# Kernel optimization log

Hardware: AMD Instinct MI355X
Metric: run time of the kernel (lower is better)

The kernel has to match this reference:

```python
import jax, jax.numpy as jnp
import numpy as np

DIM = 256; HEADS = 8; HD = 32; WS = 3; LOCAL = WS * WS; SR = 4


def _unfold(x, ws):
    # x: (B, c, H, W) -> (B, c, ws*ws, H*W), zero padding (matches nn.Unfold)
    p = ws // 2
    B, c, H, W = x.shape
    xp = jnp.pad(x, ((0, 0), (0, 0), (p, p), (p, p)))
    pat = jnp.stack([xp[:, :, i:i + H, j:j + W] for i in range(ws) for j in range(ws)], axis=2)
    return pat.reshape(B, c, ws * ws, H * W)


def _l2norm(x):
    return x / jnp.sqrt(jnp.sum(x * x, axis=-1, keepdims=True) + 1e-12)


def setup_inputs():
    key = jax.random.key(0)
    ks = jax.random.split(key, 16)
    B, H, W, C, h, d = 4, 64, 64, DIM, HEADS, HD
    N = H * W; pH, pW = H // SR, W // SR; PL = pH * pW; L = 1024
    s = 0.02
    inp = {}
    inp["x"] = jax.random.normal(ks[0], (B, N, C), jnp.float32)
    inp["relative_coords_table"] = jax.random.uniform(ks[1], (L, 2), jnp.float32, -1.0, 1.0)
    inp["relative_pos_index"] = jax.random.randint(ks[2], (N, PL), 0, L)
    inp["q_w"] = jax.random.normal(ks[3], (C, C), jnp.float32) * s
    inp["q_b"] = jnp.zeros((C,), jnp.float32)
    inp["kv_w"] = jax.random.normal(ks[4], (C, 2 * C), jnp.float32) * s
    inp["kv_b"] = jnp.zeros((2 * C,), jnp.float32)
    inp["temperature"] = jnp.log(jnp.expm1(jnp.ones((h, 1, 1), jnp.float32) / 0.24))
    inp["query_embedding"] = jax.random.normal(ks[5], (h, 1, d), jnp.float32) * s
    inp["sr_w"] = jax.random.normal(ks[6], (C, C), jnp.float32) * s
    inp["sr_b"] = jnp.zeros((C,), jnp.float32)
    inp["norm_g"] = jnp.ones((C,), jnp.float32)
    inp["norm_b"] = jnp.zeros((C,), jnp.float32)
    inp["cpb1_w"] = jax.random.normal(ks[7], (2, 512), jnp.float32) * s
    inp["cpb1_b"] = jnp.zeros((512,), jnp.float32)
    inp["cpb2_w"] = jax.random.normal(ks[8], (512, h), jnp.float32) * s
    inp["cpb2_b"] = jnp.zeros((h,), jnp.float32)
    inp["rpb_local"] = jax.random.normal(ks[9], (h, LOCAL), jnp.float32) * 0.0004
    inp["learnable_tokens"] = jax.random.normal(ks[10], (h, d, LOCAL), jnp.float32) * s
    inp["learnable_bias"] = jnp.zeros((h, 1, LOCAL), jnp.float32)
    inp["proj_w"] = jax.random.normal(ks[11], (C, C), jnp.float32) * s
    inp["proj_b"] = jnp.zeros((C,), jnp.float32)
    inp["H"] = H
    inp["W"] = W
    return inp


def _forward(x, relative_coords_table, relative_pos_index, q_w, q_b, kv_w, kv_b,
             temperature, query_embedding, sr_w, sr_b, norm_g, norm_b,
             cpb1_w, cpb1_b, cpb2_w, cpb2_b, rpb_local, learnable_tokens,
             learnable_bias, proj_w, proj_b, H, W):
    B, N, C = x.shape
    h, d = HEADS, HD
    pH, pW = H // SR, W // SR
    PL = pH * pW

    # static buffers: per-pixel valid-neighbor count, log seq-length scale, padding mask
    uf1 = _unfold(jnp.ones((1, 1, H, W), jnp.float32), WS)[0, 0]   # (LOCAL, N)
    counts = uf1.sum(axis=0)[:, None]                               # (N, 1)
    seq_scale = jnp.log(counts + PL)                                # (N, 1)
    pad_mask = (uf1.T == 0)                                         # (N, LOCAL)

    q = (x @ q_w + q_b).reshape(B, N, h, d).transpose(0, 2, 1, 3)   # (B,h,N,d)
    q_norm = _l2norm(q)
    q_scaled = (q_norm + query_embedding) * jax.nn.softplus(temperature) * seq_scale

    kv = (x @ kv_w + kv_b).reshape(B, N, 2 * h, d).transpose(0, 2, 1, 3)
    k_local, v_local = kv[:, :h], kv[:, h:]                         # (B,h,N,d)

    # --- local branch: sliding-window QK^T + learned relative bias ---
    kn = _l2norm(k_local)
    k_img = kn.transpose(0, 1, 3, 2).reshape(B, h * d, H, W)
    k_uf = _unfold(k_img, WS).reshape(B, h, d, LOCAL, N)            # (B,h,d,l,N)
    attn_local = jnp.einsum('bhnd,bhdln->bhnl', q_scaled, k_uf) + rpb_local[None, :, None, :]
    attn_local = jnp.where(pad_mask[None, None], jnp.float32(-1e9), attn_local)

    # --- pooled global branch ---
    xs = jax.nn.gelu(x @ sr_w + sr_b, approximate=False)            # 1x1 conv + GELU
    xs = xs.reshape(B, pH, SR, pW, SR, C).mean(axis=(2, 4)).reshape(B, PL, C)
    mu = xs.mean(-1, keepdims=True)
    var = ((xs - mu) ** 2).mean(-1, keepdims=True)
    xs = (xs - mu) / jnp.sqrt(var + 1e-5) * norm_g + norm_b         # LayerNorm

    kvp = (xs @ kv_w + kv_b).reshape(B, PL, 2 * h, d).transpose(0, 2, 1, 3)
    k_pool, v_pool = kvp[:, :h], kvp[:, h:]
    kp = _l2norm(k_pool)

    # MLP-generated continuous relative position bias
    t = jax.nn.relu(relative_coords_table @ cpb1_w + cpb1_b) @ cpb2_w + cpb2_b  # (L,h)
    pool_bias = t.T[:, relative_pos_index.reshape(-1)].reshape(h, N, PL)

    attn_pool = jnp.einsum('bhnd,bhpd->bhnp', q_scaled, kp) + pool_bias[None]

    # joint softmax over [local | pool]
    attn = jax.nn.softmax(jnp.concatenate([attn_local, attn_pool], axis=-1), axis=-1)
    attn_local, attn_pool = attn[..., :LOCAL], attn[..., LOCAL:]

    # learnable-token refinement of local weights
    attn_local = jnp.einsum('bhnd,hdl->bhnl', q_norm, learnable_tokens) + learnable_bias[None] + attn_local

    v_img = v_local.transpose(0, 1, 3, 2).reshape(B, h * d, H, W)
    v_uf = _unfold(v_img, WS).reshape(B, h, d, LOCAL, N)            # zero-padded V
    x_local = jnp.einsum('bhnl,bhdln->bhnd', attn_local, v_uf)
    x_pool = jnp.einsum('bhnp,bhpd->bhnd', attn_pool, v_pool)

    out = (x_local + x_pool).transpose(0, 2, 1, 3).reshape(B, N, C)
    return out @ proj_w + proj_b


def reference(x, relative_coords_table, relative_pos_index, q_w, q_b, kv_w, kv_b,
              temperature, query_embedding, sr_w, sr_b, norm_g, norm_b,
              cpb1_w, cpb1_b, cpb2_w, cpb2_b, rpb_local, learnable_tokens,
              learnable_bias, proj_w, proj_b, H, W):
    return _forward(x, relative_coords_table, relative_pos_index, q_w, q_b, kv_w, kv_b,
                    temperature, query_embedding, sr_w, sr_b, norm_g, norm_b,
                    cpb1_w, cpb1_b, cpb2_w, cpb2_b, rpb_local, learnable_tokens,
                    learnable_bias, proj_w, proj_b, H, W)
```

## Files before the change

kernel.cpp:

```cpp
#include <hip/hip_runtime.h>
#include <math.h>

#define B_   4
#define N_   4096
#define C_   256
#define NH   8
#define D_   32
#define PL_  256
#define IMG  64

typedef __attribute__((ext_vector_type(8))) short short8b;
typedef __attribute__((ext_vector_type(4))) float f32x4;
typedef unsigned short ushort_t;

__device__ __forceinline__ ushort_t f2bf(float f) {
    unsigned u = __float_as_uint(f);
    u += 0x7FFFu + ((u >> 16) & 1u);
    return (ushort_t)(u >> 16);
}
__device__ __forceinline__ float bf2f(ushort_t s) {
    return __uint_as_float(((unsigned)s) << 16);
}
__device__ __forceinline__ unsigned pk2(float lo, float hi) {
    return (unsigned)f2bf(lo) | ((unsigned)f2bf(hi) << 16);
}
__device__ __forceinline__ float gelu_f(float v) {
    return 0.5f * v * (1.0f + erff(v * 0.70710678118654752440f));
}

__global__ __launch_bounds__(256) void prep_all(const float* __restrict__ x,
                                                const float* __restrict__ q_w,
                                                const float* __restrict__ kv_w,
                                                const float* __restrict__ sr_w,
                                                const float* __restrict__ p_w,
                                                const float* __restrict__ rct,
                                                const float* __restrict__ c1w,
                                                const float* __restrict__ c1b,
                                                const float* __restrict__ c2w,
                                                const float* __restrict__ c2b,
                                                ushort_t* __restrict__ x_bf,
                                                ushort_t* __restrict__ WTall,
                                                ushort_t* __restrict__ pwT,
                                                float* __restrict__ tT)
{
    const int blk = blockIdx.x;
    const int tid = threadIdx.x;
    if (blk < 2048) {
        int gid = blk * 256 + tid;
        const float4* p = (const float4*)(x + (size_t)gid * 8);
        float4 v0 = p[0], v1 = p[1];
        short8b o;
        o[0]=(short)f2bf(v0.x); o[1]=(short)f2bf(v0.y);
        o[2]=(short)f2bf(v0.z); o[3]=(short)f2bf(v0.w);
        o[4]=(short)f2bf(v1.x); o[5]=(short)f2bf(v1.y);
        o[6]=(short)f2bf(v1.z); o[7]=(short)f2bf(v1.w);
        *(short8b*)&x_bf[(size_t)gid * 8] = o;
    } else if (blk < 2208) {
        int wt = (blk - 2048) * 256 + tid;
        int row = wt >> 5;
        int k0  = (wt & 31) << 3;
        const float* W; int N, n; ushort_t* dst;
        if (row < 256)       { W = q_w;  N = 256; n = row;        dst = WTall + (size_t)row * 256; }
        else if (row < 768)  { W = kv_w; N = 512; n = row - 256;  dst = WTall + (size_t)row * 256; }
        else if (row < 1024) { W = sr_w; N = 256; n = row - 768;  dst = WTall + (size_t)row * 256; }
        else                 { W = p_w;  N = 256; n = row - 1024; dst = pwT + (size_t)(row-1024) * 256; }
        short8b v;
        #pragma unroll
        for (int j = 0; j < 8; ++j) v[j] = (short)f2bf(W[(size_t)(k0 + j) * N + n]);
        *(short8b*)&dst[k0] = v;
    } else {
        int l = (blk - 2208) * 4 + (tid >> 6);
        int lane = tid & 63;
        float c0 = rct[l*2+0], c1 = rct[l*2+1];
        float acc[8] = {0,0,0,0,0,0,0,0};
        for (int j = lane; j < 512; j += 64) {
            float hv = fmaxf(c0 * c1w[j] + c1 * c1w[512+j] + c1b[j], 0.f);
            #pragma unroll
            for (int hh = 0; hh < 8; ++hh) acc[hh] += hv * c2w[j*8 + hh];
        }
        #pragma unroll
        for (int o = 32; o > 0; o >>= 1)
            #pragma unroll
            for (int hh = 0; hh < 8; ++hh) acc[hh] += __shfl_xor(acc[hh], o, 64);
        if (lane < 8) tT[lane * 1024 + l] = acc[lane] + c2b[lane];
    }
}

__global__ __launch_bounds__(256) void gemm_fused(const ushort_t* __restrict__ Abf,
                                                  const ushort_t* __restrict__ WTall,
                                                  const float* __restrict__ q_b,
                                                  const float* __restrict__ kv_b,
                                                  const float* __restrict__ sr_b,
                                                  const float* __restrict__ temp,
                                                  const float* __restrict__ qe,
                                                  ushort_t* __restrict__ qs_bf,
                                                  ushort_t* __restrict__ knv_bf,
                                                  float* __restrict__ buf_sr)
{
    __shared__ __align__(16) ushort_t Bs[64 * 256];

    const int tid  = threadIdx.x;
    const int wv   = tid >> 6;
    const int lane = tid & 63;
    const int la   = lane & 15, lg = lane >> 4;
    const int m0   = blockIdx.y * 128 + wv * 32;
    const int bx   = blockIdx.x;
    const int n0   = bx * 64;

    {
        const int srow = tid >> 2, sm = tid & 3;
        const ushort_t* wrow = WTall + (size_t)(n0 + srow) * 256;
        #pragma unroll
        for (int c8 = 0; c8 < 8; ++c8) {
            int ck = c8 * 4 + sm;
            short8b v = *(const short8b*)&wrow[ck * 8];
            *(short8b*)&Bs[srow * 256 + ((ck ^ (srow & 3)) * 8)] = v;
        }
    }
    __syncthreads();

    const ushort_t* a0p = Abf + (size_t)(m0 + la) * 256 + lg * 8;
    const ushort_t* a1p = a0p + (size_t)16 * 256;

    f32x4 acc[2][4];
    #pragma unroll
    for (int i = 0; i < 2; ++i)
        #pragma unroll
        for (int j = 0; j < 4; ++j) acc[i][j] = (f32x4){0.f, 0.f, 0.f, 0.f};

    #pragma unroll
    for (int kit = 0; kit < 8; ++kit) {
        short8b a0 = *(const short8b*)(a0p + kit * 32);
        short8b a1 = *(const short8b*)(a1p + kit * 32);
        #pragma unroll
        for (int nf = 0; nf < 4; ++nf) {
            int brow = nf * 16 + la;
            short8b bb = *(const short8b*)&Bs[brow * 256 + (((kit*4 + lg) ^ (la & 3)) * 8)];
            acc[0][nf] = __builtin_amdgcn_mfma_f32_16x16x32_bf16(a0, bb, acc[0][nf], 0, 0, 0);
            acc[1][nf] = __builtin_amdgcn_mfma_f32_16x16x32_bf16(a1, bb, acc[1][nf], 0, 0, 0);
        }
    }

    if (bx < 8) {
        const float* bias = (bx < 4) ? q_b : kv_b;
        const int cb = (bx < 4) ? n0 : (n0 - 256);
        float bv[4];
        #pragma unroll
        for (int nf = 0; nf < 4; ++nf) bv[nf] = bias[cb + nf*16 + la];
        float sp0 = 0.f, sp1 = 0.f;
        if (bx < 4) {
            sp0 = log1pf(expf(temp[bx*2 + 0]));
            sp1 = log1pf(expf(temp[bx*2 + 1]));
        }
        #pragma unroll
        for (int mf = 0; mf < 2; ++mf)
            #pragma unroll
            for (int reg = 0; reg < 4; ++reg) {
                int m = m0 + mf*16 + lg*4 + reg;
                #pragma unroll
                for (int h2 = 0; h2 < 2; ++h2) {
                    float v0 = acc[mf][2*h2][reg]   + bv[2*h2];
                    float v1 = acc[mf][2*h2+1][reg] + bv[2*h2+1];
                    float ss = v0*v0 + v1*v1;
                    ss += __shfl_xor(ss, 1, 64);
                    ss += __shfl_xor(ss, 2, 64);
                    ss += __shfl_xor(ss, 4, 64);
                    ss += __shfl_xor(ss, 8, 64);
                    float inv = rsqrtf(ss + 1e-12f);
                    if (bx < 4) {
                        int head = bx*2 + h2;
                        int n = m & (N_-1);
                        int y = n >> 6, xc = n & 63;
                        int cnt = (1 + (y > 0) + (y < IMG-1)) * (1 + (xc > 0) + (xc < IMG-1));
                        float lc = (cnt == 4) ? 5.5606816f : (cnt == 6) ? 5.5683445f : 5.5797298f;
                        float s2 = (h2 ? sp1 : sp0) * lc;
                        ushort_t* dst = qs_bf + (size_t)m * 256 + head*32;
                        dst[la]      = f2bf((v0*inv + qe[head*32 + la])      * s2);
                        dst[16 + la] = f2bf((v1*inv + qe[head*32 + 16 + la]) * s2);
                    } else {
                        int head = (bx-4)*2 + h2;
                        ushort_t* dst = knv_bf + (size_t)m * 512 + head*32;
                        dst[la]      = f2bf(v0*inv);
                        dst[16 + la] = f2bf(v1*inv);
                    }
                }
            }
    } else if (bx < 12) {
        #pragma unroll
        for (int mf = 0; mf < 2; ++mf)
            #pragma unroll
            for (int nf = 0; nf < 4; ++nf)
                #pragma unroll
                for (int reg = 0; reg < 4; ++reg) {
                    int m = m0 + mf*16 + lg*4 + reg;
                    int col_kv = n0 - 256 + nf*16 + la;
                    knv_bf[(size_t)m * 512 + col_kv] =
                        f2bf(acc[mf][nf][reg] + kv_b[col_kv]);
                }
    } else {
        #pragma unroll
        for (int mf = 0; mf < 2; ++mf)
            #pragma unroll
            for (int nf = 0; nf < 4; ++nf)
                #pragma unroll
                for (int reg = 0; reg < 4; ++reg) {
                    int m = m0 + mf*16 + lg*4 + reg;
                    int c = n0 + nf*16 + la - 768;
                    buf_sr[(size_t)m * 256 + c] = gelu_f(acc[mf][nf][reg] + sr_b[c]);
                }
    }
}

__global__ __launch_bounds__(256) void gemm_kvp(const ushort_t* __restrict__ Abf,
                                                const ushort_t* __restrict__ WT,
                                                const float* __restrict__ kv_b,
                                                ushort_t* __restrict__ kp_bf,
                                                ushort_t* __restrict__ vpT_bf)
{
    __shared__ __align__(16) ushort_t Bs[64 * 256];

    const int tid  = threadIdx.x;
    const int wv   = tid >> 6;
    const int lane = tid & 63;
    const int la   = lane & 15, lg = lane >> 4;
    const int m0   = blockIdx.y * 128 + wv * 32;
    const int bx   = blockIdx.x;
    const int n0   = bx * 64;

    {
        const int srow = tid >> 2, sm = tid & 3;
        const ushort_t* wrow = WT + (size_t)(n0 + srow) * 256;
        #pragma unroll
        for (int c8 = 0; c8 < 8; ++c8) {
            int ck = c8 * 4 + sm;
            short8b v = *(const short8b*)&wrow[ck * 8];
            *(short8b*)&Bs[srow * 256 + ((ck ^ (srow & 3)) * 8)] = v;
        }
    }
    __syncthreads();

    const ushort_t* a0p = Abf + (size_t)(m0 + la) * 256 + lg * 8;
    const ushort_t* a1p = a0p + (size_t)16 * 256;

    f32x4 acc[2][4];
    #pragma unroll
    for (int i = 0; i < 2; ++i)
        #pragma unroll
        for (int j = 0; j < 4; ++j) acc[i][j] = (f32x4){0.f, 0.f, 0.f, 0.f};

    #pragma unroll
    for (int kit = 0; kit < 8; ++kit) {
        short8b a0 = *(const short8b*)(a0p + kit * 32);
        short8b a1 = *(const short8b*)(a1p + kit * 32);
        #pragma unroll
        for (int nf = 0; nf < 4; ++nf) {
            int brow = nf * 16 + la;
            short8b bb = *(const short8b*)&Bs[brow * 256 + (((kit*4 + lg) ^ (la & 3)) * 8)];
            acc[0][nf] = __builtin_amdgcn_mfma_f32_16x16x32_bf16(a0, bb, acc[0][nf], 0, 0, 0);
            acc[1][nf] = __builtin_amdgcn_mfma_f32_16x16x32_bf16(a1, bb, acc[1][nf], 0, 0, 0);
        }
    }

    if (bx < 4) {
        float bv[4];
        #pragma unroll
        for (int nf = 0; nf < 4; ++nf) bv[nf] = kv_b[n0 + nf*16 + la];
        #pragma unroll
        for (int mf = 0; mf < 2; ++mf)
            #pragma unroll
            for (int reg = 0; reg < 4; ++reg) {
                int m = m0 + mf*16 + lg*4 + reg;
                int b = m >> 8, p = m & 255;
                #pragma unroll
                for (int h2 = 0; h2 < 2; ++h2) {
                    float v0 = acc[mf][2*h2][reg]   + bv[2*h2];
                    float v1 = acc[mf][2*h2+1][reg] + bv[2*h2+1];
                    float ss = v0*v0 + v1*v1;
                    ss += __shfl_xor(ss, 1, 64);
                    ss += __shfl_xor(ss, 2, 64);
                    ss += __shfl_xor(ss, 4, 64);
                    ss += __shfl_xor(ss, 8, 64);
                    float inv = rsqrtf(ss + 1e-12f);
                    int head = bx*2 + h2;
                    ushort_t* dst = kp_bf + (((size_t)(b*NH + head)) * PL_ + p) * 32;
                    dst[la]      = f2bf(v0*inv);
                    dst[16 + la] = f2bf(v1*inv);
                }
            }
    } else {
        #pragma unroll
        for (int mf = 0; mf < 2; ++mf)
            #pragma unroll
            for (int nf = 0; nf < 4; ++nf)
                #pragma unroll
                for (int reg = 0; reg < 4; ++reg) {
                    int m = m0 + mf*16 + lg*4 + reg;
                    int b = m >> 8, p = m & 255;
                    int col_kv = n0 + nf*16 + la;
                    int cv = col_kv - 256;
                    int head = cv >> 5, d = cv & 31;
                    vpT_bf[(((size_t)(b*NH + head)) * 32 + d) * 256 + p] =
                        f2bf(acc[mf][nf][reg] + kv_b[col_kv]);
                }
    }
}

template<int ACT>
__global__ __launch_bounds__(256) void gemm_mfma(const ushort_t* __restrict__ Abf,
                                                 const ushort_t* __restrict__ WT,
                                                 const float* __restrict__ bias,
                                                 float* __restrict__ out,
                                                 int M, int N)
{
    __shared__ __align__(16) ushort_t Bs[64 * 256];

    const int tid  = threadIdx.x;
    const int wv   = tid >> 6;
    const int lane = tid & 63;
    const int la   = lane & 15, lg = lane >> 4;
    const int m0   = blockIdx.y * 128 + wv * 32;
    const int n0   = blockIdx.x * 64;

    {
        const int srow = tid >> 2, sm = tid & 3;
        const ushort_t* wrow = WT + (size_t)(n0 + srow) * 256;
        #pragma unroll
        for (int c8 = 0; c8 < 8; ++c8) {
            int ck = c8 * 4 + sm;
            short8b v = *(const short8b*)&wrow[ck * 8];
            *(short8b*)&Bs[srow * 256 + ((ck ^ (srow & 3)) * 8)] = v;
        }
    }
    __syncthreads();

    const ushort_t* a0p = Abf + (size_t)(m0 + la) * 256 + lg * 8;
    const ushort_t* a1p = a0p + (size_t)16 * 256;

    f32x4 acc[2][4];
    #pragma unroll
    for (int i = 0; i < 2; ++i)
        #pragma unroll
        for (int j = 0; j < 4; ++j) acc[i][j] = (f32x4){0.f, 0.f, 0.f, 0.f};

    #pragma unroll
    for (int kit = 0; kit < 8; ++kit) {
        short8b a0 = *(const short8b*)(a0p + kit * 32);
        short8b a1 = *(const short8b*)(a1p + kit * 32);
        #pragma unroll
        for (int nf = 0; nf < 4; ++nf) {
            int brow = nf * 16 + la;
            short8b bb = *(const short8b*)&Bs[brow * 256 + (((kit*4 + lg) ^ (la & 3)) * 8)];
            acc[0][nf] = __builtin_amdgcn_mfma_f32_16x16x32_bf16(a0, bb, acc[0][nf], 0, 0, 0);
            acc[1][nf] = __builtin_amdgcn_mfma_f32_16x16x32_bf16(a1, bb, acc[1][nf], 0, 0, 0);
        }
    }
    #pragma unroll
    for (int mf = 0; mf < 2; ++mf)
        #pragma unroll
        for (int nf = 0; nf < 4; ++nf)
            #pragma unroll
            for (int reg = 0; reg < 4; ++reg) {
                int m  = m0 + mf * 16 + lg * 4 + reg;
                int nn = n0 + nf * 16 + la;
                float v = acc[mf][nf][reg] + bias[nn];
                if (ACT == 1) v = gelu_f(v);
                out[(size_t)m * N + nn] = v;
            }
}

__global__ __launch_bounds__(256) void mid_prep(const int* __restrict__ rpi,
                                                const float* __restrict__ tT,
                                                const ushort_t* __restrict__ knv,
                                                const float* __restrict__ sr,
                                                const float* __restrict__ g,
                                                const float* __restrict__ bb,
                                                ushort_t* __restrict__ pbl,
                                                ushort_t* __restrict__ xs,
                                                ushort_t* __restrict__ vT)
{
    __shared__ float red[256];
    __shared__ __align__(16) ushort_t ts[256][40];
    const int blk = blockIdx.x;
    const int tid = threadIdx.x;

    if (blk < 8192) {
        int gid = blk * 256 + tid;
        int la   = gid & 15;
        int lg   = (gid >> 4) & 3;
        int t    = (gid >> 6) & 15;
        int wv   = (gid >> 10) & 3;
        int tile = (gid >> 12) & 63;
        int h    = gid >> 18;
        int n  = tile * 64 + wv * 16 + la;
        int p0 = t * 16 + lg * 4;
        int4 r = *(const int4*)&rpi[(size_t)n * PL_ + p0];
        const float* tTh = tT + h * 1024;
        ushort4 o;
        o.x = f2bf(tTh[r.x]);
        o.y = f2bf(tTh[r.y]);
        o.z = f2bf(tTh[r.z]);
        o.w = f2bf(tTh[r.w]);
        *(ushort4*)&pbl[(size_t)gid * 4] = o;
    } else if (blk < 9216) {
        int bp = blk - 8192;
        int b = bp >> 8, p = bp & 255;
        int i0 = p >> 4, j0 = p & 15;
        int c = tid;
        float s = 0.f;
        #pragma unroll
        for (int di = 0; di < 4; ++di)
            #pragma unroll
            for (int dj = 0; dj < 4; ++dj) {
                int n = (i0*4 + di) * IMG + (j0*4 + dj);
                s += sr[((size_t)b * N_ + n) * C_ + c];
            }
        s *= (1.f / 16.f);
        red[c] = s; __syncthreads();
        for (int o = 128; o > 0; o >>= 1) { if (c < o) red[c] += red[c+o]; __syncthreads(); }
        float mean = red[0] * (1.f/256.f);
        __syncthreads();
        float dcen = s - mean;
        red[c] = dcen * dcen; __syncthreads();
        for (int o = 128; o > 0; o >>= 1) { if (c < o) red[c] += red[c+o]; __syncthreads(); }
        float var = red[0] * (1.f/256.f);
        float outv = dcen * rsqrtf(var + 1e-5f) * g[c] + bb[c];
        xs[(size_t)bp * C_ + c] = f2bf(outv);
    } else {
        int vb = blk - 9216;
        int nt = vb & 15, bh = vb >> 4;
        const ushort_t* src = knv + ((size_t)((bh >> 3)*N_ + nt*256 + tid)) * 512 + 256 + (bh & 7)*32;
        #pragma unroll
        for (int c = 0; c < 4; ++c)
            *(short8b*)&ts[tid][c*8] = *(const short8b*)&src[c*8];
        __syncthreads();
        int d = tid >> 3, cc = tid & 7;
        ushort_t* dst = vT + ((size_t)bh*32 + d) * (size_t)N_ + nt*256;
        #pragma unroll
        for (int k = 0; k < 4; ++k) {
            int n0 = cc*32 + k*8;
            short8b v;
            #pragma unroll
            for (int j = 0; j < 8; ++j) v[j] = ts[n0+j][d];
            *(short8b*)&dst[n0] = v;
        }
    }
}

__global__ __launch_bounds__(256) void attn_v4(
    const ushort_t* __restrict__ qs_g,
    const ushort_t* __restrict__ knv_g,
    const ushort_t* __restrict__ kp_g,
    const ushort_t* __restrict__ vpT_g,
    const ushort_t* __restrict__ vT_g,
    const ushort_t* __restrict__ pbl,
    const float* __restrict__ rpb,
    const float* __restrict__ qe,
    const float* __restrict__ temp,
    const float* __restrict__ lt,
    const float* __restrict__ lb,
    ushort_t* __restrict__ outp)
{
    __shared__ __align__(16) ushort_t qs_lds[64*32];
    __shared__ __align__(16) ushort_t ltT_lds[16*32];
    __shared__ __align__(16) ushort_t Wb_lds[4*3*16*40];
    __shared__ float wloc[64*10];
    __shared__ float wext[64*10];
    __shared__ float invs2[64];
    __shared__ float rpb_lds[9], elb_lds[9];

    const int tile = blockIdx.x;
    const int hh   = blockIdx.y;
    const int b    = blockIdx.z;
    const int tid  = threadIdx.x;
    const int wv   = tid >> 6;
    const int lane = tid & 63;
    const int la   = lane & 15;
    const int lg   = lane >> 4;
    const int r0   = wv * 16;

    {
        int row = tid >> 2, ck = tid & 3;
        short8b v = *(const short8b*)&qs_g[((size_t)(b*N_ + tile*64 + row)) * 256 + hh*32 + ck*8];
        *(short8b*)&qs_lds[row*32 + ((ck ^ (row & 3)) * 8)] = v;
    }
    {
        int l = tid >> 4, dd = (tid & 15) * 2;
        ushort_t a = (l < 9) ? f2bf(lt[hh*288 + dd*9 + l]) : (ushort_t)0;
        ushort_t c = (l < 9) ? f2bf(lt[hh*288 + (dd+1)*9 + l]) : (ushort_t)0;
        ltT_lds[l*32 + dd]   = a;
        ltT_lds[l*32 + dd+1] = c;
    }
    {
        short8b z = {0,0,0,0,0,0,0,0};
        for (int i = tid; i < 960; i += 256) *(short8b*)&Wb_lds[i*8] = z;
    }
    if (tid < 64) {
        int xx = tid;
        int ci = 1 + (tile > 0) + (tile < IMG-1);
        int cj = 1 + (xx > 0) + (xx < IMG-1);
        float sp = log1pf(expf(temp[hh]));
        invs2[tid] = 1.0f / (sp * logf((float)(ci*cj) + (float)PL_));
    }
    if (tid >= 64 && tid < 73) {
        int l = tid - 64;
        float e = 0.f;
        for (int d = 0; d < 32; ++d) e += qe[hh*32 + d] * lt[hh*288 + d*9 + l];
        elb_lds[l] = lb[hh*9 + l] - e;
        rpb_lds[l] = rpb[hh*9 + l];
    }
    __syncthreads();

    const short8b af = *(const short8b*)&qs_lds[(r0+la)*32 + ((lg ^ (la & 3)) * 8)];

    {
        f32x4 G[3][2];
        const f32x4 zc = {0.f,0.f,0.f,0.f};
        #pragma unroll
        for (int dyi = 0; dyi < 3; ++dyi) {
            int cy = tile + dyi - 1;
            cy = cy < 0 ? 0 : (cy > 63 ? 63 : cy);
            #pragma unroll
            for (int f = 0; f < 2; ++f) {
                int xp = wv*16 - 8 + 16*f + la;
                xp = xp < 0 ? 0 : (xp > 63 ? 63 : xp);
                const short8b kf = *(const short8b*)
                    &knv_g[((size_t)(b*N_ + cy*64 + xp)) * 512 + hh*32 + lg*8];
                G[dyi][f] = __builtin_amdgcn_mfma_f32_16x16x32_bf16(af, kf, zc, 0, 0, 0);
            }
        }
        #pragma unroll
        for (int f = 0; f < 2; ++f)
            #pragma unroll
            for (int reg = 0; reg < 4; ++reg) {
                int r  = lg*4 + reg;
                int dx = la + 16*f - 8 - r;
                if (dx >= -1 && dx <= 1) {
                    #pragma unroll
                    for (int dyi = 0; dyi < 3; ++dyi)
                        wloc[(r0 + r)*10 + dyi*3 + dx + 1] = G[dyi][f][reg];
                }
            }
    }

    {
        const short8b ltf = *(const short8b*)&ltT_lds[la*32 + lg*8];
        const f32x4 zc = {0.f,0.f,0.f,0.f};
        f32x4 E = __builtin_amdgcn_mfma_f32_16x16x32_bf16(af, ltf, zc, 0, 0, 0);
        if (la < 9) {
            #pragma unroll
            for (int reg = 0; reg < 4; ++reg) {
                int rr = r0 + lg*4 + reg;
                wext[rr*10 + la] = invs2[rr] * E[reg] + elb_lds[la];
            }
        }
    }

    const ushort_t* kph = kp_g + ((size_t)(b*NH + hh) * PL_) * 32;
    const ushort_t* pbw = pbl + ((((size_t)hh * 64 + tile) * 4 + wv) * 4096);

    f32x4 acc[16];
    #pragma unroll
    for (int t = 0; t < 16; ++t) {
        ushort4 b4 = *(const ushort4*)&pbw[t*256 + lg*64 + la*4];
        f32x4 c;
        c[0] = bf2f(b4.x); c[1] = bf2f(b4.y); c[2] = bf2f(b4.z); c[3] = bf2f(b4.w);
        short8b kf = *(const short8b*)&kph[(t*16 + la)*32 + lg*8];
        acc[t] = __builtin_amdgcn_mfma_f32_16x16x32_bf16(kf, af, c, 0, 0, 0);
    }

    const int rr = r0 + la;
    float mx = -3.0e38f;
    #pragma unroll
    for (int t = 0; t < 16; ++t)
        #pragma unroll
        for (int reg = 0; reg < 4; ++reg) mx = fmaxf(mx, acc[t][reg]);
    mx = fmaxf(mx, __shfl_xor(mx, 16, 64));
    mx = fmaxf(mx, __shfl_xor(mx, 32, 64));
    float lv[9];
    #pragma unroll
    for (int l = 0; l < 9; ++l) {
        int dy = l/3 - 1, dx = l%3 - 1;
        int yy = tile + dy, xx = rr + dx;
        bool val = (yy >= 0 && yy < IMG && xx >= 0 && xx < IMG);
        lv[l] = val ? (wloc[rr*10 + l] + rpb_lds[l]) : -1e9f;
        mx = fmaxf(mx, lv[l]);
    }

    float s = 0.f;
    #pragma unroll
    for (int t = 0; t < 16; ++t)
        #pragma unroll
        for (int reg = 0; reg < 4; ++reg) {
            float e = __expf(acc[t][reg] - mx);
            acc[t][reg] = e;
            s += e;
        }
    s += __shfl_xor(s, 16, 64);
    s += __shfl_xor(s, 32, 64);
    float sl = 0.f;
    float el[9];
    #pragma unroll
    for (int l = 0; l < 9; ++l) { el[l] = __expf(lv[l] - mx); sl += el[l]; }
    s += sl;
    const float inv = 1.f / s;

    if (lg == 0) {
        #pragma unroll
        for (int l = 0; l < 9; ++l) {
            int dy = l/3 - 1, dx = l%3 - 1;
            int yy = tile + dy, xx = rr + dx;
            bool val = (yy >= 0 && yy < IMG && xx >= 0 && xx < IMG);
            float wl = el[l]*inv + wext[rr*10 + l];
            Wb_lds[((wv*3 + l/3)*16 + la)*40 + (la + 8 + dx)] =
                val ? f2bf(wl) : (ushort_t)0;
        }
    }

    f32x4 o0 = {0.f,0.f,0.f,0.f}, o1 = {0.f,0.f,0.f,0.f};

    {
        const ushort_t* vTh = vT_g + (size_t)(b*NH + hh) * 32 * N_;
        #pragma unroll
        for (int dyi = 0; dyi < 3; ++dyi) {
            int cy = tile + dyi - 1;
            cy = cy < 0 ? 0 : (cy > 63 ? 63 : cy);
            int nb = cy*64 + wv*16 - 8 + lg*8;
            nb = nb < 0 ? 0 : (nb > (N_ - 8) ? (N_ - 8) : nb);
            short8b wf = *(const short8b*)&Wb_lds[((wv*3 + dyi)*16 + la)*40 + lg*8];
            short8b vf0 = *(const short8b*)&vTh[(size_t)la * N_ + nb];
            short8b vf1 = *(const short8b*)&vTh[(size_t)(16 + la) * N_ + nb];
            o0 = __builtin_amdgcn_mfma_f32_16x16x32_bf16(wf, vf0, o0, 0, 0, 0);
            o1 = __builtin_amdgcn_mfma_f32_16x16x32_bf16(wf, vf1, o1, 0, 0, 0);
        }
    }

    {
        const int src0 = la + 32*(lg & 1);
        const int src1 = src0 + 16;
        const bool hi  = (lg >= 2);
        const ushort_t* vph = vpT_g + ((size_t)(b*NH + hh) * 32) * 256;
        #pragma unroll
        for (int kk = 0; kk < 8; ++kk) {
            unsigned A0 = pk2(acc[2*kk][0]*inv,   acc[2*kk][1]*inv);
            unsigned A1 = pk2(acc[2*kk][2]*inv,   acc[2*kk][3]*inv);
            unsigned B0 = pk2(acc[2*kk+1][0]*inv, acc[2*kk+1][1]*inv);
            unsigned B1 = pk2(acc[2*kk+1][2]*inv, acc[2*kk+1][3]*inv);
            unsigned xa0 = __shfl(A0, src0, 64), xb0 = __shfl(B0, src0, 64);
            unsigned xa1 = __shfl(A1, src0, 64), xb1 = __shfl(B1, src0, 64);
            unsigned ya0 = __shfl(A0, src1, 64), yb0 = __shfl(B0, src1, 64);
            unsigned ya1 = __shfl(A1, src1, 64), yb1 = __shfl(B1, src1, 64);
            union { unsigned u[4]; short8b v; } wf;
            wf.u[0] = hi ? xb0 : xa0;
            wf.u[1] = hi ? xb1 : xa1;
            wf.u[2] = hi ? yb0 : ya0;
            wf.u[3] = hi ? yb1 : ya1;
            short8b vf0 = *(const short8b*)&vph[(size_t)la*256      + kk*32 + lg*8];
            short8b vf1 = *(const short8b*)&vph[(size_t)(16+la)*256 + kk*32 + lg*8];
            o0 = __builtin_amdgcn_mfma_f32_16x16x32_bf16(wf.v, vf0, o0, 0, 0, 0);
            o1 = __builtin_amdgcn_mfma_f32_16x16x32_bf16(wf.v, vf1, o1, 0, 0, 0);
        }
    }

    #pragma unroll
    for (int reg = 0; reg < 4; ++reg) {
        int r2 = r0 + lg*4 + reg;
        int n  = tile*64 + r2;
        ushort_t* orow = outp + ((size_t)(b*N_ + n)) * C_ + hh*32;
        orow[la]      = f2bf(o0[reg]);
        orow[16 + la] = f2bf(o1[reg]);
    }
}

extern "C" void kernel_launch(void* const* d_in, const int* in_sizes, int n_in,
                              void* d_out, int out_size, void* d_ws, size_t ws_size,
                              hipStream_t stream) {
    const float* x    = (const float*)d_in[0];
    const float* rct  = (const float*)d_in[1];
    const int*   rpi  = (const int*)  d_in[2];
    const float* q_w  = (const float*)d_in[3];
    const float* q_b  = (const float*)d_in[4];
    const float* kv_w = (const float*)d_in[5];
    const float* kv_b = (const float*)d_in[6];
    const float* temp = (const float*)d_in[7];
    const float* qe   = (const float*)d_in[8];
    const float* sr_w = (const float*)d_in[9];
    const float* sr_b = (const float*)d_in[10];
    const float* ng   = (const float*)d_in[11];
    const float* nb   = (const float*)d_in[12];
    const float* c1w  = (const float*)d_in[13];
    const float* c1b  = (const float*)d_in[14];
    const float* c2w  = (const float*)d_in[15];
    const float* c2b  = (const float*)d_in[16];
    const float* rpb  = (const float*)d_in[17];
    const float* lt   = (const float*)d_in[18];
    const float* lb   = (const float*)d_in[19];
    const float* p_w  = (const float*)d_in[20];
    const float* p_b  = (const float*)d_in[21];
    float* out = (float*)d_out;

    float* ws = (float*)d_ws;
    const size_t MN = (size_t)B_ * N_;
    float* buf_sr  = ws;
    float* buf_t   = buf_sr + MN * 256;
    ushort_t* x_bf   = (ushort_t*)(buf_t + 8*1024);
    ushort_t* pre_bf = x_bf   + MN * 256;
    ushort_t* WTall  = pre_bf + MN * 256;
    ushort_t* pwT    = WTall  + 1024*256;
    ushort_t* qs_bf  = pwT    + 256*256;
    ushort_t* knv_bf = qs_bf  + MN * 256;
    ushort_t* kp_bf  = knv_bf + MN * 512;
    ushort_t* vpT_bf = kp_bf  + (size_t)B_*NH*PL_*32;
    ushort_t* vT_bf  = vpT_bf + (size_t)B_*NH*32*PL_;
    ushort_t* pbl    = vT_bf  + (size_t)B_*NH*32*N_;
    ushort_t* xs_bf  = pbl    + (size_t)2097152*4;

    const int M = (int)MN;

    prep_all<<<2464, 256, 0, stream>>>(x, q_w, kv_w, sr_w, p_w, rct,
                                       c1w, c1b, c2w, c2b, x_bf, WTall, pwT, buf_t);
    gemm_fused<<<dim3(16, M/128), 256, 0, stream>>>(x_bf, WTall, q_b, kv_b, sr_b,
                                                    temp, qe, qs_bf, knv_bf, buf_sr);
    mid_prep<<<9728, 256, 0, stream>>>(rpi, buf_t, knv_bf, buf_sr, ng, nb,
                                       pbl, xs_bf, vT_bf);
    gemm_kvp<<<dim3(8, 8), 256, 0, stream>>>(xs_bf, WTall + 256*256, kv_b,
                                             kp_bf, vpT_bf);
    attn_v4<<<dim3(64, 8, 4), 256, 0, stream>>>(qs_bf, knv_bf, kp_bf, vpT_bf, vT_bf,
                                                pbl, rpb, qe, temp, lt, lb, pre_bf);
    gemm_mfma<0><<<dim3(4, M/128), 256, 0, stream>>>(pre_bf, pwT, p_b, out, M, 256);
}
```

Measured before the change: 131.6 us.

## Move bias gather into QKV GEMM launch and remap attention block order

The relative-position bias gather (pbl), which only depends on rpi and the CPB table, moves out of mid_prep into extra blocks appended to the gemm_fused grid. Those memory-bound blocks can then overlap with the compute-bound GEMM blocks instead of running in a separate phase. Separately, attention blocks are launched as a 1D grid with a swizzled mapping that spreads consecutive block IDs across tiles, heads and batches, probably to balance XCD or L2 locality. The gather blocks still allocate the GEMM's 32KB of LDS, which may limit how many of them fit per CU.

```diff
diff --git a/kernel.cpp b/kernel.cpp
--- a/kernel.cpp
+++ b/kernel.cpp
@@ -93,6 +93,9 @@
                                                   const float* __restrict__ sr_b,
                                                   const float* __restrict__ temp,
                                                   const float* __restrict__ qe,
+                                                  const int* __restrict__ rpi,
+                                                  const float* __restrict__ tT,
+                                                  ushort_t* __restrict__ pbl,
                                                   ushort_t* __restrict__ qs_bf,
                                                   ushort_t* __restrict__ knv_bf,
                                                   float* __restrict__ buf_sr)
@@ -100,6 +103,29 @@
     __shared__ __align__(16) ushort_t Bs[64 * 256];
 
     const int tid  = threadIdx.x;
+
+    if (blockIdx.y >= 128) {
+        int pbid = (blockIdx.y - 128) * 16 + blockIdx.x;
+        int gid = pbid * 256 + tid;
+        int la   = gid & 15;
+        int lg   = (gid >> 4) & 3;
+        int t    = (gid >> 6) & 15;
+        int wv   = (gid >> 10) & 3;
+        int tile = (gid >> 12) & 63;
+        int h    = gid >> 18;
+        int n  = tile * 64 + wv * 16 + la;
+        int p0 = t * 16 + lg * 4;
+        int4 r = *(const int4*)&rpi[(size_t)n * PL_ + p0];
+        const float* tTh = tT + h * 1024;
+        ushort4 o;
+        o.x = f2bf(tTh[r.x]);
+        o.y = f2bf(tTh[r.y]);
+        o.z = f2bf(tTh[r.z]);
+        o.w = f2bf(tTh[r.w]);
+        *(ushort4*)&pbl[(size_t)gid * 4] = o;
+        return;
+    }
+
     const int wv   = tid >> 6;
     const int lane = tid & 63;
     const int la   = lane & 15, lg = lane >> 4;
@@ -368,13 +394,10 @@
             }
 }
 
-__global__ __launch_bounds__(256) void mid_prep(const int* __restrict__ rpi,
-                                                const float* __restrict__ tT,
-                                                const ushort_t* __restrict__ knv,
+__global__ __launch_bounds__(256) void mid_prep(const ushort_t* __restrict__ knv,
                                                 const float* __restrict__ sr,
                                                 const float* __restrict__ g,
                                                 const float* __restrict__ bb,
-                                                ushort_t* __restrict__ pbl,
                                                 ushort_t* __restrict__ xs,
                                                 ushort_t* __restrict__ vT)
 {
@@ -383,26 +406,8 @@
     const int blk = blockIdx.x;
     const int tid = threadIdx.x;
 
-    if (blk < 8192) {
-        int gid = blk * 256 + tid;
-        int la   = gid & 15;
-        int lg   = (gid >> 4) & 3;
-        int t    = (gid >> 6) & 15;
-        int wv   = (gid >> 10) & 3;
-        int tile = (gid >> 12) & 63;
-        int h    = gid >> 18;
-        int n  = tile * 64 + wv * 16 + la;
-        int p0 = t * 16 + lg * 4;
-        int4 r = *(const int4*)&rpi[(size_t)n * PL_ + p0];
-        const float* tTh = tT + h * 1024;
-        ushort4 o;
-        o.x = f2bf(tTh[r.x]);
-        o.y = f2bf(tTh[r.y]);
-        o.z = f2bf(tTh[r.z]);
-        o.w = f2bf(tTh[r.w]);
-        *(ushort4*)&pbl[(size_t)gid * 4] = o;
-    } else if (blk < 9216) {
-        int bp = blk - 8192;
+    if (blk < 1024) {
+        int bp = blk;
         int b = bp >> 8, p = bp & 255;
         int i0 = p >> 4, j0 = p & 15;
         int c = tid;
@@ -426,7 +431,7 @@
         float outv = dcen * rsqrtf(var + 1e-5f) * g[c] + bb[c];
         xs[(size_t)bp * C_ + c] = f2bf(outv);
     } else {
-        int vb = blk - 9216;
+        int vb = blk - 1024;
         int nt = vb & 15, bh = vb >> 4;
         const ushort_t* src = knv + ((size_t)((bh >> 3)*N_ + nt*256 + tid)) * 512 + 256 + (bh & 7)*32;
         #pragma unroll
@@ -468,9 +473,12 @@
     __shared__ float invs2[64];
     __shared__ float rpb_lds[9], elb_lds[9];
 
-    const int tile = blockIdx.x;
-    const int hh   = blockIdx.y;
-    const int b    = blockIdx.z;
+    const int lin  = blockIdx.x;
+    const int virt = (lin & 7) * 256 + (lin >> 3);
+    const int tile = virt & 63;
+    const int hh   = (virt >> 6) & 7;
+    const int b    = virt >> 9;
+
     const int tid  = threadIdx.x;
     const int wv   = tid >> 6;
     const int lane = tid & 63;
@@ -718,13 +726,13 @@
 
     prep_all<<<2464, 256, 0, stream>>>(x, q_w, kv_w, sr_w, p_w, rct,
                                        c1w, c1b, c2w, c2b, x_bf, WTall, pwT, buf_t);
-    gemm_fused<<<dim3(16, M/128), 256, 0, stream>>>(x_bf, WTall, q_b, kv_b, sr_b,
-                                                    temp, qe, qs_bf, knv_bf, buf_sr);
-    mid_prep<<<9728, 256, 0, stream>>>(rpi, buf_t, knv_bf, buf_sr, ng, nb,
-                                       pbl, xs_bf, vT_bf);
+    gemm_fused<<<dim3(16, 128 + 512), 256, 0, stream>>>(x_bf, WTall, q_b, kv_b, sr_b,
+                                                        temp, qe, rpi, buf_t, pbl,
+                                                        qs_bf, knv_bf, buf_sr);
+    mid_prep<<<1536, 256, 0, stream>>>(knv_bf, buf_sr, ng, nb, xs_bf, vT_bf);
     gemm_kvp<<<dim3(8, 8), 256, 0, stream>>>(xs_bf, WTall + 256*256, kv_b,
                                              kp_bf, vpT_bf);
-    attn_v4<<<dim3(64, 8, 4), 256, 0, stream>>>(qs_bf, knv_bf, kp_bf, vpT_bf, vT_bf,
-                                                pbl, rpb, qe, temp, lt, lb, pre_bf);
+    attn_v4<<<2048, 256, 0, stream>>>(qs_bf, knv_bf, kp_bf, vpT_bf, vT_bf,
+                                      pbl, rpb, qe, temp, lt, lb, pre_bf);
     gemm_mfma<0><<<dim3(4, M/128), 256, 0, stream>>>(pre_bf, pwT, p_b, out, M, 256);
 }
```

After: 130.8 us. About the same (-0.6%).
